# Kernel optimization log

Hardware: AMD Instinct MI355X
Metric: run time of the kernel (lower is better)

Reference implementation:

```python
import jax, jax.numpy as jnp
import numpy as np
import math

T, B, D = 1024, 256, 64
E, H, L = 512, 256, 4


def setup_inputs() -> dict:
    key = jax.random.key(0)
    ks = jax.random.split(key, 10)
    x_sequence = jax.random.normal(ks[0], (T, B, D), dtype=jnp.float32)
    seq_lengths = jax.random.randint(ks[1], (B,), 1, T)
    # create_b_mask: ones in first half of dims, zeros in second half
    b_mask = jnp.concatenate([jnp.ones((1, D // 2)), jnp.zeros((1, D // 2))], axis=1).astype(jnp.float32)
    W_in = jax.random.normal(ks[2], (L, D + E, H), dtype=jnp.float32) / np.sqrt(D + E)
    b_in = jnp.zeros((L, H), dtype=jnp.float32)
    W_s = jax.random.normal(ks[3], (L, H, D), dtype=jnp.float32) / np.sqrt(H)
    b_s = jnp.zeros((L, D), dtype=jnp.float32)
    W_t = jax.random.normal(ks[4], (L, H, D), dtype=jnp.float32) / np.sqrt(H)
    b_t = jnp.zeros((L, D), dtype=jnp.float32)
    rescale_w = jnp.ones((1, D), dtype=jnp.float32)
    # ESN reservoir (fixed random), scaled for spectral stability under tanh
    W_res = jax.random.normal(ks[5], (E, E), dtype=jnp.float32) * (0.9 / np.sqrt(E))
    W_inp = jax.random.normal(ks[6], (D, E), dtype=jnp.float32) * 0.1
    return dict(x_sequence=x_sequence, seq_lengths=seq_lengths, b_mask=b_mask,
                W_in=W_in, b_in=b_in, W_s=W_s, b_s=b_s, W_t=W_t, b_t=b_t,
                rescale_w=rescale_w, W_res=W_res, W_inp=W_inp)


def _forward(x_sequence, seq_lengths, b_mask, W_in, b_in, W_s, b_s, W_t, b_t,
             rescale_w, W_res, W_inp):
    Tlen, Bsz, Dd = x_sequence.shape
    log2pi = jnp.asarray(math.log(2.0 * math.pi), dtype=x_sequence.dtype)

    def nn_apply(xm, h_esn, l):
        # small conditioning MLP: concat(masked frame, esn state) -> hidden -> (slope, intercept)
        inp = jnp.concatenate([xm, h_esn], axis=1)           # (B, D+E)
        hid = jnp.tanh(inp @ W_in[l] + b_in[l])              # (B, H)
        slope = jnp.tanh(hid @ W_s[l] + b_s[l]) * rescale_w  # (B, D), rescaled
        intercept = hid @ W_t[l] + b_t[l]                    # (B, D)
        return slope, intercept

    def f_inverse(z, m, h_esn, l):
        slope, intercept = nn_apply(m * z, h_esn, l)
        z_new = m * z + (1.0 - m) * ((z - intercept) * jnp.exp(-slope))
        log_det = slope @ (m.T - 1.0)                        # (B, 1)
        return z_new, log_det

    def loglike_frame(x_frame, h_esn):
        ll = jnp.zeros((Bsz, 1), dtype=x_frame.dtype)
        z = x_frame
        for l in reversed(range(L)):  # small fixed loop over flow layers
            z, ld = f_inverse(z, 1.0 - b_mask, h_esn, l)
            ll = ll + ld
            z, ld = f_inverse(z, b_mask, h_esn, l)
            ll = ll + ld
        ll = ll - 0.5 * jnp.sum(z * z, axis=1, keepdims=True) - 0.5 * Dd * log2pi
        return ll

    def step(carry, inp):
        h_esn, ll_seq = carry
        t, x_frame = inp
        lf = loglike_frame(x_frame, h_esn)
        length_mask = (t < seq_lengths).astype(lf.dtype)[:, None]  # (B,1)
        ll_seq = ll_seq + lf * length_mask
        h_esn = jnp.tanh(h_esn @ W_res.T + x_frame @ W_inp)        # ESN update
        return (h_esn, ll_seq), None

    h0 = jnp.zeros((Bsz, W_res.shape[0]), dtype=x_sequence.dtype)
    ll0 = jnp.zeros((Bsz, 1), dtype=x_sequence.dtype)
    ts = jnp.arange(Tlen)
    (h_final, ll_seq), _ = jax.lax.scan(step, (h0, ll0), (ts, x_sequence))
    return ll_seq  # (B, 1)


def reference(x_sequence, seq_lengths, b_mask, W_in, b_in, W_s, b_s, W_t, b_t,
              rescale_w, W_res, W_inp):
    return _forward(x_sequence, seq_lengths, b_mask, W_in, b_in, W_s, b_s,
                    W_t, b_t, rescale_w, W_res, W_inp)
```

## Files before the change

kernel.cpp:

```cpp
#include <hip/hip_runtime.h>

#define T_LEN 1024
#define B_SZ  256
#define D_DIM 64
#define E_DIM 512
#define H_DIM 256

#define SA 552
#define SH 264
#define SF 66
#define ROWB 1152

using short8 = __attribute__((ext_vector_type(8))) short;
using half8  = __attribute__((ext_vector_type(8))) _Float16;
using f32x4  = __attribute__((ext_vector_type(4))) float;
typedef unsigned long long ull;

static __device__ __forceinline__ unsigned short f2bf(float v) {
    unsigned u = __float_as_uint(v);
    u += 0x7FFFu + ((u >> 16) & 1u);
    return (unsigned short)(u >> 16);
}
static __device__ __forceinline__ unsigned short f2h(float v) {
    _Float16 h = (_Float16)v;
    unsigned short u;
    __builtin_memcpy(&u, &h, 2);
    return u;
}
static __device__ __forceinline__ float h2f(unsigned short u) {
    _Float16 h;
    __builtin_memcpy(&h, &u, 2);
    return (float)h;
}
static __device__ __forceinline__ float fast_tanh(float x) {
    x = fminf(15.f, fmaxf(-15.f, x));
    float e = __expf(2.f * x);
    return (e - 1.f) / (e + 1.f);
}
static __device__ __forceinline__ int rswz(int row, int byte_in_row) {
    return row * ROWB + (byte_in_row ^ ((row & 7) << 4));
}

__global__ void prep_kernel(const float* __restrict__ W_in, const float* __restrict__ W_s,
                            const float* __restrict__ W_t, const float* __restrict__ W_res,
                            const float* __restrict__ W_inp, const float* __restrict__ x_seq,
                            unsigned short* __restrict__ W_inF, unsigned short* __restrict__ W_stF,
                            unsigned short* __restrict__ W_packo, unsigned short* __restrict__ x_h) {
    int idx = blockIdx.x * blockDim.x + threadIdx.x;
    int stride = gridDim.x * blockDim.x;
    const int total1 = 8 * 16 * 17 * 64 * 8;
    for (int i = idx; i < total1; i += stride) {
        int j    = i & 7;
        int lane = (i >> 3) & 63;
        int ks   = (i >> 9) % 17;
        int nt   = (i / (512 * 17)) & 15;
        int ls   = i / (512 * 17 * 16);
        int side = ls & 1, l = ls >> 1;
        int n = nt * 16 + (lane & 15);
        int k = ks * 32 + (lane >> 4) * 8 + j;
        int ksrc = (k < 32) ? (side == 0 ? 32 + k : k) : (k + 32);
        W_inF[i] = f2bf(W_in[(l * 576 + ksrc) * H_DIM + n]);
    }
    const int total2 = 8 * 4 * 8 * 64 * 8;
    for (int i = idx; i < total2; i += stride) {
        int j    = i & 7;
        int lane = (i >> 3) & 63;
        int ks   = (i >> 9) & 7;
        int nt   = (i >> 12) & 3;
        int ls   = i >> 14;
        int side = ls & 1, l = ls >> 1;
        int nst = nt * 16 + (lane & 15);
        int k   = ks * 32 + (lane >> 4) * 8 + j;
        int j32 = nst & 31;
        int d   = side ? (32 + j32) : j32;
        float v = (nst < 32) ? W_s[(l * H_DIM + k) * D_DIM + d] : W_t[(l * H_DIM + k) * D_DIM + d];
        W_stF[i] = f2bf(v);
    }
    const int total3 = E_DIM * 576;
    for (int i = idx; i < total3; i += stride) {
        int k = i % 576;
        int n = i / 576;
        float v = (k < E_DIM) ? W_res[n * E_DIM + k] : W_inp[(k - E_DIM) * E_DIM + n];
        W_packo[i] = f2h(v);
    }
    const int total4 = T_LEN * B_SZ * D_DIM;
    for (int i = idx; i < total4; i += stride)
        x_h[i] = f2h(x_seq[i]);
}

__launch_bounds__(256, 1)
__global__ void esn_kernel(const unsigned short* __restrict__ x_h,
                           const unsigned short* __restrict__ W_pack,
                           unsigned short* __restrict__ h_store ,
                           unsigned short* __restrict__ h_buf   ,
                           unsigned int* __restrict__ ctr,
                           int t0, int tc) {
    const int bid  = blockIdx.x;
    const int g    = bid & 15;
    const int m    = bid >> 4;
    const int tid  = threadIdx.x;
    const int wave = tid >> 6;
    const int lane = tid & 63;
    const int arow = lane & 15;
    const int kq   = lane >> 4;
    const int r0   = g * 16;
    const int n0   = m * 64;
    const size_t HB = (size_t)B_SZ * E_DIM;
    unsigned int* gctr = ctr + g * 32;

    extern __shared__ char smem[];
    char* Wlb = smem;
    char* hAb = smem + 64 * ROWB;

    {
        const int r  = tid & 63;
        const int c0 = (tid >> 6) * 18;
        #pragma unroll
        for (int u = 0; u < 18; ++u) {
            const int byte = 16 * (c0 + u);
            *reinterpret_cast<uint4*>(Wlb + rswz(r, byte)) =
                *reinterpret_cast<const uint4*>(
                    reinterpret_cast<const char*>(&W_pack[(size_t)(n0 + r) * 576]) + byte);
        }
    }

    const int srow = tid >> 4;
    const int seg  = tid & 15;
    const int xrow = tid >> 2, xc = tid & 3;

    for (int tl = 0; tl < tc; ++tl) {
        const int t = t0 + tl;
        const unsigned short* hb_r = h_buf + (size_t)(t & 1) * HB;
        unsigned short*       hb_w = h_buf + (size_t)((t & 1) ^ 1) * HB;

        uint4 xa = {0,0,0,0}, xb = {0,0,0,0};
        if (tid < 64) {
            const unsigned short* xp = &x_h[((size_t)t * B_SZ + r0 + xrow) * D_DIM + xc * 16];
            xa = *reinterpret_cast<const uint4*>(xp);
            xb = *reinterpret_cast<const uint4*>(xp + 8);
        }

        if (tid == 0) {
            while (__hip_atomic_fetch_add(gctr, 0u, __ATOMIC_RELAXED,
                                          __HIP_MEMORY_SCOPE_AGENT) < 8u * (unsigned)t)
                __builtin_amdgcn_s_sleep(1);
        }
        __syncthreads();
        asm volatile("" ::: "memory");

        ull hv[8];
        const ull* hrow = reinterpret_cast<const ull*>(&hb_r[(size_t)(r0 + srow) * E_DIM]);
        #pragma unroll
        for (int q = 0; q < 4; ++q) {
            const int c = seg + 16 * q;
            hv[2*q]   = __hip_atomic_load(hrow + 2*c,     __ATOMIC_RELAXED, __HIP_MEMORY_SCOPE_SYSTEM);
            hv[2*q+1] = __hip_atomic_load(hrow + 2*c + 1, __ATOMIC_RELAXED, __HIP_MEMORY_SCOPE_SYSTEM);
        }
        #pragma unroll
        for (int q = 0; q < 4; ++q) {
            const int c = seg + 16 * q;
            uint4 pk;
            __builtin_memcpy(&pk, &hv[2*q], 16);
            *reinterpret_cast<uint4*>(hAb + rswz(srow, 16 * c)) = pk;
        }
        if (tid < 64) {
            *reinterpret_cast<uint4*>(hAb + rswz(xrow, 1024 + 32 * xc))      = xa;
            *reinterpret_cast<uint4*>(hAb + rswz(xrow, 1024 + 32 * xc + 16)) = xb;
        }
        __syncthreads();

        if (tl == 0) {
            #pragma unroll
            for (int q = 0; q < 4; ++q) {
                const int c = seg + 16 * q;
                unsigned short o[8];
                #pragma unroll
                for (int j = 0; j < 4; ++j) o[j]     = f2bf(h2f((unsigned short)(hv[2*q]   >> (16 * j))));
                #pragma unroll
                for (int j = 0; j < 4; ++j) o[4 + j] = f2bf(h2f((unsigned short)(hv[2*q+1] >> (16 * j))));
                uint4 pk;
                __builtin_memcpy(&pk, o, 16);
                *reinterpret_cast<uint4*>(&h_store[(size_t)(r0 + srow) * E_DIM + 8 * c]) = pk;
            }
        }

        f32x4 accA = (f32x4){0.f, 0.f, 0.f, 0.f};
        f32x4 accB = (f32x4){0.f, 0.f, 0.f, 0.f};
        #pragma unroll
        for (int ks = 0; ks < 18; ++ks) {
            half8 a = *reinterpret_cast<const half8*>(hAb + rswz(arow, ks * 64 + kq * 16));
            half8 b = *reinterpret_cast<const half8*>(Wlb + rswz(wave * 16 + arow, ks * 64 + kq * 16));
            if (ks & 1) accB = __builtin_amdgcn_mfma_f32_16x16x32_f16(a, b, accB, 0, 0, 0);
            else        accA = __builtin_amdgcn_mfma_f32_16x16x32_f16(a, b, accA, 0, 0, 0);
        }
        f32x4 acc = accA + accB;

        const int ncol = n0 + wave * 16 + arow;
        #pragma unroll
        for (int i = 0; i < 4; ++i) {
            const int row = r0 + kq * 4 + i;
            float hvf = fast_tanh(acc[i]);
            __hip_atomic_store(&hb_w[(size_t)row * E_DIM + ncol], f2h(hvf),
                               __ATOMIC_RELAXED, __HIP_MEMORY_SCOPE_SYSTEM);
            if (tl + 1 < tc)
                h_store[((size_t)(tl + 1) * B_SZ + row) * E_DIM + ncol] = f2bf(hvf);
        }

        asm volatile("s_waitcnt vmcnt(0)" ::: "memory");
        __syncthreads();
        if (tid == 0)
            __hip_atomic_fetch_add(gctr, 1u, __ATOMIC_RELAXED, __HIP_MEMORY_SCOPE_AGENT);
    }
}

__launch_bounds__(256, 2)
__global__ void flow_kernel(const float* __restrict__ x_seq, const unsigned short* __restrict__ h_store,
                            const unsigned short* __restrict__ W_inF, const unsigned short* __restrict__ W_stF,
                            const float* __restrict__ b_in, const float* __restrict__ b_s,
                            const float* __restrict__ b_t, const float* __restrict__ rescale_w,
                            const int* __restrict__ seq_len, float* __restrict__ ll_part,
                            int t0, int tc) {
    const int tt   = blockIdx.x >> 4;
    const int bt   = blockIdx.x & 15;
    const int tid  = threadIdx.x;
    const int wave = tid >> 6;
    const int lane = tid & 63;

    __shared__ unsigned short abf[32 * SA];
    __shared__ unsigned short hidbf[32 * SH];
    __shared__ float zf[32][D_DIM];
    __shared__ float llacc[32];
    __shared__ float llb[16];
    float* stf = reinterpret_cast<float*>(hidbf);

    if (tid < 16) llb[tid] = 0.f;

    const int r8 = tid >> 3;
    const int c8 = tid & 7;

    for (int s = 0; s < 8; ++s) {
        const int trow = tt * 16 + 2 * s + (r8 >> 4);
        const int brow = bt * 16 + (r8 & 15);
        {
            const float* xp = &x_seq[((size_t)(t0 + trow) * B_SZ + brow) * D_DIM + c8 * 8];
            float4 v0 = *reinterpret_cast<const float4*>(xp);
            float4 v1 = *reinterpret_cast<const float4*>(xp + 4);
            *reinterpret_cast<float4*>(&zf[r8][c8 * 8])     = v0;
            *reinterpret_cast<float4*>(&zf[r8][c8 * 8 + 4]) = v1;
            const unsigned short* hp = &h_store[((size_t)trow * B_SZ + brow) * E_DIM + c8 * 64];
            unsigned short* ap = &abf[r8 * SA + 32 + c8 * 64];
            #pragma unroll
            for (int q = 0; q < 8; ++q)
                *reinterpret_cast<uint4*>(ap + q * 8) = *reinterpret_cast<const uint4*>(hp + q * 8);
        }
        if (tid < 32) llacc[tid] = 0.f;
        __syncthreads();

        for (int stage = 0; stage < 8; ++stage) {
            const int l = 3 - (stage >> 1);
            const int side = stage & 1;
            const int ls = l * 2 + side;
            {
                #pragma unroll
                for (int q = 0; q < 4; ++q) {
                    int k = c8 * 4 + q;
                    int d = side ? k : (32 + k);
                    abf[r8 * SA + k] = f2bf(zf[r8][d]);
                }
            }
            __syncthreads();

            const unsigned short* wbase =
                W_inF + ((size_t)(ls * 16 + wave * 4) * 17) * 512 + lane * 8;
            f32x4 acc[2][4];
            #pragma unroll
            for (int mt = 0; mt < 2; ++mt)
                #pragma unroll
                for (int nt = 0; nt < 4; ++nt)
                    acc[mt][nt] = (f32x4){0.f, 0.f, 0.f, 0.f};
            const int aoff = (lane & 15) * SA + 8 * (lane >> 4);
            short8 bb[6][4];
            #pragma unroll
            for (int p = 0; p < 6; ++p)
                #pragma unroll
                for (int nt = 0; nt < 4; ++nt)
                    bb[p][nt] = *reinterpret_cast<const short8*>(wbase + (size_t)nt * 8704 + p * 512);
            #pragma unroll
            for (int ks = 0; ks < 17; ++ks) {
                const int k0 = ks * 32;
                short8 a0 = *reinterpret_cast<const short8*>(&abf[aoff + k0]);
                short8 a1 = *reinterpret_cast<const short8*>(&abf[16 * SA + aoff + k0]);
                #pragma unroll
                for (int nt = 0; nt < 4; ++nt) {
                    acc[0][nt] = __builtin_amdgcn_mfma_f32_16x16x32_bf16(a0, bb[ks % 6][nt], acc[0][nt], 0, 0, 0);
                    acc[1][nt] = __builtin_amdgcn_mfma_f32_16x16x32_bf16(a1, bb[ks % 6][nt], acc[1][nt], 0, 0, 0);
                }
                if (ks + 6 < 17) {
                    #pragma unroll
                    for (int nt = 0; nt < 4; ++nt)
                        bb[ks % 6][nt] = *reinterpret_cast<const short8*>(
                            wbase + (size_t)nt * 8704 + (ks + 6) * 512);
                }
            }
            #pragma unroll
            for (int mt = 0; mt < 2; ++mt)
                #pragma unroll
                for (int nt = 0; nt < 4; ++nt) {
                    const int n = wave * 64 + nt * 16 + (lane & 15);
                    const float bias = b_in[l * H_DIM + n];
                    #pragma unroll
                    for (int i = 0; i < 4; ++i) {
                        const int row = mt * 16 + (lane >> 4) * 4 + i;
                        hidbf[row * SH + n] = f2bf(fast_tanh(acc[mt][nt][i] + bias));
                    }
                }
            __syncthreads();

            const unsigned short* wstb =
                W_stF + ((size_t)(ls * 4 + wave) * 8) * 512 + lane * 8;
            f32x4 acc2[2];
            acc2[0] = (f32x4){0.f,0.f,0.f,0.f};
            acc2[1] = (f32x4){0.f,0.f,0.f,0.f};
            const int hoff = (lane & 15) * SH + 8 * (lane >> 4);
            const int nst  = wave * 16 + (lane & 15);
            short8 bs0 = *reinterpret_cast<const short8*>(wstb);
            #pragma unroll
            for (int ks = 0; ks < 8; ++ks) {
                short8 bcur = bs0;
                if (ks + 1 < 8) bs0 = *reinterpret_cast<const short8*>(wstb + (ks + 1) * 512);
                const int k0 = ks * 32;
                short8 a0 = *reinterpret_cast<const short8*>(&hidbf[hoff + k0]);
                short8 a1 = *reinterpret_cast<const short8*>(&hidbf[16 * SH + hoff + k0]);
                acc2[0] = __builtin_amdgcn_mfma_f32_16x16x32_bf16(a0, bcur, acc2[0], 0, 0, 0);
                acc2[1] = __builtin_amdgcn_mfma_f32_16x16x32_bf16(a1, bcur, acc2[1], 0, 0, 0);
            }
            __syncthreads();
            {
                const int j = nst & 31;
                const int d = side ? (32 + j) : j;
                const bool is_s = (nst < 32);
                const float bias = is_s ? b_s[l * D_DIM + d] : b_t[l * D_DIM + d];
                const float rs = rescale_w[d];
                #pragma unroll
                for (int mt = 0; mt < 2; ++mt)
                    #pragma unroll
                    for (int i = 0; i < 4; ++i) {
                        const int row = mt * 16 + (lane >> 4) * 4 + i;
                        const float v = acc2[mt][i] + bias;
                        stf[row * SF + nst] = is_s ? (fast_tanh(v) * rs) : v;
                    }
            }
            __syncthreads();
            {
                float p = 0.f;
                #pragma unroll
                for (int q = 0; q < 4; ++q) {
                    const int j = c8 * 4 + q;
                    const int d = side ? (32 + j) : j;
                    const float sv = stf[r8 * SF + j];
                    const float iv = stf[r8 * SF + 32 + j];
                    zf[r8][d] = (zf[r8][d] - iv) * __expf(-sv);
                    p += sv;
                }
                p += __shfl_xor(p, 1);
                p += __shfl_xor(p, 2);
                p += __shfl_xor(p, 4);
                if (c8 == 0) llacc[r8] -= p;
            }
            __syncthreads();
        }

        {
            float zs = 0.f;
            #pragma unroll
            for (int q = 0; q < 8; ++q) {
                float z = zf[r8][c8 * 8 + q];
                zs += z * z;
            }
            zs += __shfl_xor(zs, 1);
            zs += __shfl_xor(zs, 2);
            zs += __shfl_xor(zs, 4);
            if (c8 == 0) {
                float ll = llacc[r8] - 0.5f * zs - 58.812066125f;
                llacc[r8] = ((t0 + trow) < seq_len[brow]) ? ll : 0.f;
            }
        }
        __syncthreads();
        if (tid < 16) llb[tid] += llacc[tid] + llacc[16 + tid];
        __syncthreads();
    }

    if (tid < 16)
        ll_part[((t0 >> 4) + tt) * B_SZ + bt * 16 + tid] = llb[tid];
}

__global__ void reduce_kernel(const float* __restrict__ ll_part, float* __restrict__ out) {
    int b = threadIdx.x;
    float s = 0.f;
    #pragma unroll
    for (int tt = 0; tt < T_LEN / 16; ++tt) s += ll_part[tt * B_SZ + b];
    out[b] = s;
}

extern "C" void kernel_launch(void* const* d_in, const int* in_sizes, int n_in,
                              void* d_out, int out_size, void* d_ws, size_t ws_size,
                              hipStream_t stream) {
    const float* x_seq   = (const float*)d_in[0];
    const int*   seqlen  = (const int*)d_in[1];
    const float* W_in    = (const float*)d_in[3];
    const float* b_in    = (const float*)d_in[4];
    const float* W_s     = (const float*)d_in[5];
    const float* b_s     = (const float*)d_in[6];
    const float* W_t     = (const float*)d_in[7];
    const float* b_t     = (const float*)d_in[8];
    const float* rescale = (const float*)d_in[9];
    const float* W_res   = (const float*)d_in[10];
    const float* W_inp   = (const float*)d_in[11];

    char* ws = (char*)d_ws;
    size_t off = 0;
    unsigned short* W_inF  = (unsigned short*)(ws + off); off += (size_t)8 * 16 * 17 * 64 * 8 * 2;
    unsigned short* W_stF  = (unsigned short*)(ws + off); off += (size_t)8 * 4 * 8 * 64 * 8 * 2;
    unsigned short* W_pack = (unsigned short*)(ws + off); off += (size_t)E_DIM * 576 * 2;
    unsigned short* x_h    = (unsigned short*)(ws + off); off += (size_t)T_LEN * B_SZ * D_DIM * 2;
    float* ll_part = (float*)(ws + off); off += (size_t)(T_LEN / 16) * B_SZ * 4;
    unsigned short* h_buf  = (unsigned short*)(ws + off); off += (size_t)2 * B_SZ * E_DIM * 2;
    unsigned int* ctr = (unsigned int*)(ws + off); off += (size_t)16 * 32 * 4;
    unsigned short* h_store = (unsigned short*)(ws + off);

    size_t per_t = (size_t)B_SZ * E_DIM * 2;
    size_t rem = (ws_size > off) ? (ws_size - off) : 0;
    long long tcl = (long long)(rem / per_t);
    int tc = (int)((tcl > T_LEN) ? T_LEN : tcl);
    tc &= ~15;
    if (tc < 16) tc = 16;

    hipMemsetAsync(h_buf, 0, (size_t)2 * B_SZ * E_DIM * 2, stream);
    hipMemsetAsync(ctr, 0, (size_t)16 * 32 * 4, stream);

    prep_kernel<<<2048, 256, 0, stream>>>(W_in, W_s, W_t, W_res, W_inp, x_seq,
                                          W_inF, W_stF, W_pack, x_h);
    const int esn_lds = (64 + 16) * ROWB;
    for (int t0 = 0; t0 < T_LEN; t0 += tc) {
        int cur = T_LEN - t0; if (cur > tc) cur = tc;
        esn_kernel<<<128, 256, esn_lds, stream>>>(x_h, W_pack, h_store, h_buf, ctr, t0, cur);
        flow_kernel<<<(cur / 16) * 16, 256, 0, stream>>>(x_seq, h_store, W_inF, W_stF, b_in, b_s, b_t,
                                                         rescale, seqlen, ll_part, t0, cur);
    }
    reduce_kernel<<<1, B_SZ, 0, stream>>>(ll_part, (float*)d_out);
}
```

Measured before the change: 3.851 ms.

## Process 64 rows per flow-kernel iteration to amortize weight fetches

Result: slower. 4.833 ms (+25.5%).

```diff
diff --git a/kernel.cpp b/kernel.cpp
--- a/kernel.cpp
+++ b/kernel.cpp
@@ -10,6 +10,8 @@
 #define SH 264
 #define SF 66
 #define ROWB 1152
+
+#define FLOW_LDS (64*SA*2 + 64*SH*2 + 64*64*4 + 64*4 + 16*4)
 
 using short8 = __attribute__((ext_vector_type(8))) short;
 using half8  = __attribute__((ext_vector_type(8))) _Float16;
@@ -213,7 +215,7 @@
     }
 }
 
-__launch_bounds__(256, 2)
+__launch_bounds__(256, 1)
 __global__ void flow_kernel(const float* __restrict__ x_seq, const unsigned short* __restrict__ h_store,
                             const unsigned short* __restrict__ W_inF, const unsigned short* __restrict__ W_stF,
                             const float* __restrict__ b_in, const float* __restrict__ b_s,
@@ -226,34 +228,35 @@
     const int wave = tid >> 6;
     const int lane = tid & 63;
 
-    __shared__ unsigned short abf[32 * SA];
-    __shared__ unsigned short hidbf[32 * SH];
-    __shared__ float zf[32][D_DIM];
-    __shared__ float llacc[32];
-    __shared__ float llb[16];
-    float* stf = reinterpret_cast<float*>(hidbf);
+    extern __shared__ char smemf[];
+    unsigned short* abf   = reinterpret_cast<unsigned short*>(smemf);
+    unsigned short* hidbf = abf + 64 * SA;
+    float* zf    = reinterpret_cast<float*>(hidbf + 64 * SH);
+    float* llacc = zf + 64 * 64;
+    float* llb   = llacc + 64;
+    float* stf   = reinterpret_cast<float*>(hidbf);
 
     if (tid < 16) llb[tid] = 0.f;
 
-    const int r8 = tid >> 3;
-    const int c8 = tid & 7;
-
-    for (int s = 0; s < 8; ++s) {
-        const int trow = tt * 16 + 2 * s + (r8 >> 4);
-        const int brow = bt * 16 + (r8 & 15);
+    const int row4 = tid >> 2;
+    const int c4   = tid & 3;
+
+    for (int s = 0; s < 4; ++s) {
+        const int trow = tt * 16 + 4 * s + (row4 >> 4);
+        const int brow = bt * 16 + (row4 & 15);
         {
-            const float* xp = &x_seq[((size_t)(t0 + trow) * B_SZ + brow) * D_DIM + c8 * 8];
-            float4 v0 = *reinterpret_cast<const float4*>(xp);
-            float4 v1 = *reinterpret_cast<const float4*>(xp + 4);
-            *reinterpret_cast<float4*>(&zf[r8][c8 * 8])     = v0;
-            *reinterpret_cast<float4*>(&zf[r8][c8 * 8 + 4]) = v1;
-            const unsigned short* hp = &h_store[((size_t)trow * B_SZ + brow) * E_DIM + c8 * 64];
-            unsigned short* ap = &abf[r8 * SA + 32 + c8 * 64];
-            #pragma unroll
-            for (int q = 0; q < 8; ++q)
+            const float* xp = &x_seq[((size_t)(t0 + trow) * B_SZ + brow) * D_DIM + c4 * 16];
+            #pragma unroll
+            for (int q = 0; q < 4; ++q)
+                *reinterpret_cast<float4*>(&zf[row4 * 64 + c4 * 16 + q * 4]) =
+                    *reinterpret_cast<const float4*>(xp + q * 4);
+            const unsigned short* hp = &h_store[((size_t)trow * B_SZ + brow) * E_DIM + c4 * 128];
+            unsigned short* ap = &abf[row4 * SA + 32 + c4 * 128];
+            #pragma unroll
+            for (int q = 0; q < 16; ++q)
                 *reinterpret_cast<uint4*>(ap + q * 8) = *reinterpret_cast<const uint4*>(hp + q * 8);
         }
-        if (tid < 32) llacc[tid] = 0.f;
+        if (tid < 64) llacc[tid] = 0.f;
         __syncthreads();
 
         for (int stage = 0; stage < 8; ++stage) {
@@ -262,19 +265,19 @@
             const int ls = l * 2 + side;
             {
                 #pragma unroll
-                for (int q = 0; q < 4; ++q) {
-                    int k = c8 * 4 + q;
+                for (int q = 0; q < 8; ++q) {
+                    int k = c4 * 8 + q;
                     int d = side ? k : (32 + k);
-                    abf[r8 * SA + k] = f2bf(zf[r8][d]);
+                    abf[row4 * SA + k] = f2bf(zf[row4 * 64 + d]);
                 }
             }
             __syncthreads();
 
             const unsigned short* wbase =
                 W_inF + ((size_t)(ls * 16 + wave * 4) * 17) * 512 + lane * 8;
-            f32x4 acc[2][4];
-            #pragma unroll
-            for (int mt = 0; mt < 2; ++mt)
+            f32x4 acc[4][4];
+            #pragma unroll
+            for (int mt = 0; mt < 4; ++mt)
                 #pragma unroll
                 for (int nt = 0; nt < 4; ++nt)
                     acc[mt][nt] = (f32x4){0.f, 0.f, 0.f, 0.f};
@@ -288,13 +291,15 @@
             #pragma unroll
             for (int ks = 0; ks < 17; ++ks) {
                 const int k0 = ks * 32;
-                short8 a0 = *reinterpret_cast<const short8*>(&abf[aoff + k0]);
-                short8 a1 = *reinterpret_cast<const short8*>(&abf[16 * SA + aoff + k0]);
-                #pragma unroll
-                for (int nt = 0; nt < 4; ++nt) {
-                    acc[0][nt] = __builtin_amdgcn_mfma_f32_16x16x32_bf16(a0, bb[ks % 6][nt], acc[0][nt], 0, 0, 0);
-                    acc[1][nt] = __builtin_amdgcn_mfma_f32_16x16x32_bf16(a1, bb[ks % 6][nt], acc[1][nt], 0, 0, 0);
-                }
+                short8 am[4];
+                #pragma unroll
+                for (int mt = 0; mt < 4; ++mt)
+                    am[mt] = *reinterpret_cast<const short8*>(&abf[mt * 16 * SA + aoff + k0]);
+                #pragma unroll
+                for (int nt = 0; nt < 4; ++nt)
+                    #pragma unroll
+                    for (int mt = 0; mt < 4; ++mt)
+                        acc[mt][nt] = __builtin_amdgcn_mfma_f32_16x16x32_bf16(am[mt], bb[ks % 6][nt], acc[mt][nt], 0, 0, 0);
                 if (ks + 6 < 17) {
                     #pragma unroll
                     for (int nt = 0; nt < 4; ++nt)
@@ -303,24 +308,24 @@
                 }
             }
             #pragma unroll
-            for (int mt = 0; mt < 2; ++mt)
-                #pragma unroll
-                for (int nt = 0; nt < 4; ++nt) {
-                    const int n = wave * 64 + nt * 16 + (lane & 15);
-                    const float bias = b_in[l * H_DIM + n];
+            for (int nt = 0; nt < 4; ++nt) {
+                const int n = wave * 64 + nt * 16 + (lane & 15);
+                const float bias = b_in[l * H_DIM + n];
+                #pragma unroll
+                for (int mt = 0; mt < 4; ++mt)
                     #pragma unroll
                     for (int i = 0; i < 4; ++i) {
                         const int row = mt * 16 + (lane >> 4) * 4 + i;
                         hidbf[row * SH + n] = f2bf(fast_tanh(acc[mt][nt][i] + bias));
                     }
-                }
+            }
             __syncthreads();
 
             const unsigned short* wstb =
                 W_stF + ((size_t)(ls * 4 + wave) * 8) * 512 + lane * 8;
-            f32x4 acc2[2];
-            acc2[0] = (f32x4){0.f,0.f,0.f,0.f};
-            acc2[1] = (f32x4){0.f,0.f,0.f,0.f};
+            f32x4 acc2[4];
+            #pragma unroll
+            for (int mt = 0; mt < 4; ++mt) acc2[mt] = (f32x4){0.f, 0.f, 0.f, 0.f};
             const int hoff = (lane & 15) * SH + 8 * (lane >> 4);
             const int nst  = wave * 16 + (lane & 15);
             short8 bs0 = *reinterpret_cast<const short8*>(wstb);
@@ -329,10 +334,11 @@
                 short8 bcur = bs0;
                 if (ks + 1 < 8) bs0 = *reinterpret_cast<const short8*>(wstb + (ks + 1) * 512);
                 const int k0 = ks * 32;
-                short8 a0 = *reinterpret_cast<const short8*>(&hidbf[hoff + k0]);
-                short8 a1 = *reinterpret_cast<const short8*>(&hidbf[16 * SH + hoff + k0]);
-                acc2[0] = __builtin_amdgcn_mfma_f32_16x16x32_bf16(a0, bcur, acc2[0], 0, 0, 0);
-                acc2[1] = __builtin_amdgcn_mfma_f32_16x16x32_bf16(a1, bcur, acc2[1], 0, 0, 0);
+                #pragma unroll
+                for (int mt = 0; mt < 4; ++mt) {
+                    short8 a = *reinterpret_cast<const short8*>(&hidbf[mt * 16 * SH + hoff + k0]);
+                    acc2[mt] = __builtin_amdgcn_mfma_f32_16x16x32_bf16(a, bcur, acc2[mt], 0, 0, 0);
+                }
             }
             __syncthreads();
             {
@@ -342,7 +348,7 @@
                 const float bias = is_s ? b_s[l * D_DIM + d] : b_t[l * D_DIM + d];
                 const float rs = rescale_w[d];
                 #pragma unroll
-                for (int mt = 0; mt < 2; ++mt)
+                for (int mt = 0; mt < 4; ++mt)
                     #pragma unroll
                     for (int i = 0; i < 4; ++i) {
                         const int row = mt * 16 + (lane >> 4) * 4 + i;
@@ -354,18 +360,17 @@
             {
                 float p = 0.f;
                 #pragma unroll
-                for (int q = 0; q < 4; ++q) {
-                    const int j = c8 * 4 + q;
+                for (int q = 0; q < 8; ++q) {
+                    const int j = c4 * 8 + q;
                     const int d = side ? (32 + j) : j;
-                    const float sv = stf[r8 * SF + j];
-                    const float iv = stf[r8 * SF + 32 + j];
-                    zf[r8][d] = (zf[r8][d] - iv) * __expf(-sv);
+                    const float sv = stf[row4 * SF + j];
+                    const float iv = stf[row4 * SF + 32 + j];
+                    zf[row4 * 64 + d] = (zf[row4 * 64 + d] - iv) * __expf(-sv);
                     p += sv;
                 }
                 p += __shfl_xor(p, 1);
                 p += __shfl_xor(p, 2);
-                p += __shfl_xor(p, 4);
-                if (c8 == 0) llacc[r8] -= p;
+                if (c4 == 0) llacc[row4] -= p;
             }
             __syncthreads();
         }
@@ -373,20 +378,20 @@
         {
             float zs = 0.f;
             #pragma unroll
-            for (int q = 0; q < 8; ++q) {
-                float z = zf[r8][c8 * 8 + q];
+            for (int q = 0; q < 16; ++q) {
+                float z = zf[row4 * 64 + c4 * 16 + q];
                 zs += z * z;
             }
             zs += __shfl_xor(zs, 1);
             zs += __shfl_xor(zs, 2);
-            zs += __shfl_xor(zs, 4);
-            if (c8 == 0) {
-                float ll = llacc[r8] - 0.5f * zs - 58.812066125f;
-                llacc[r8] = ((t0 + trow) < seq_len[brow]) ? ll : 0.f;
-            }
-        }
-        __syncthreads();
-        if (tid < 16) llb[tid] += llacc[tid] + llacc[16 + tid];
+            if (c4 == 0) {
+                float ll = llacc[row4] - 0.5f * zs - 58.812066125f;
+                llacc[row4] = ((t0 + trow) < seq_len[brow]) ? ll : 0.f;
+            }
+        }
+        __syncthreads();
+        if (tid < 16)
+            llb[tid] += llacc[tid] + llacc[16 + tid] + llacc[32 + tid] + llacc[48 + tid];
         __syncthreads();
     }
 
@@ -444,8 +449,9 @@
     for (int t0 = 0; t0 < T_LEN; t0 += tc) {
         int cur = T_LEN - t0; if (cur > tc) cur = tc;
         esn_kernel<<<128, 256, esn_lds, stream>>>(x_h, W_pack, h_store, h_buf, ctr, t0, cur);
-        flow_kernel<<<(cur / 16) * 16, 256, 0, stream>>>(x_seq, h_store, W_inF, W_stF, b_in, b_s, b_t,
-                                                         rescale, seqlen, ll_part, t0, cur);
+        flow_kernel<<<(cur / 16) * 16, 256, FLOW_LDS, stream>>>(x_seq, h_store, W_inF, W_stF,
+                                                                b_in, b_s, b_t, rescale, seqlen,
+                                                                ll_part, t0, cur);
     }
     reduce_kernel<<<1, B_SZ, 0, stream>>>(ll_part, (float*)d_out);
 }
```

## Restructure flow kernel to process four row-groups per stage and keep z in registers

Applied to the files above, without the earlier changes.

Result: slower. 4.005 ms (+4.0%).

```diff
diff --git a/kernel.cpp b/kernel.cpp
--- a/kernel.cpp
+++ b/kernel.cpp
@@ -10,6 +10,8 @@
 #define SH 264
 #define SF 66
 #define ROWB 1152
+
+#define FLOW_LDS (128*SA*2 + 32*SH*2 + 128*4)
 
 using short8 = __attribute__((ext_vector_type(8))) short;
 using half8  = __attribute__((ext_vector_type(8))) _Float16;
@@ -213,63 +215,68 @@
     }
 }
 
-__launch_bounds__(256, 2)
+__launch_bounds__(256, 1)
 __global__ void flow_kernel(const float* __restrict__ x_seq, const unsigned short* __restrict__ h_store,
                             const unsigned short* __restrict__ W_inF, const unsigned short* __restrict__ W_stF,
                             const float* __restrict__ b_in, const float* __restrict__ b_s,
                             const float* __restrict__ b_t, const float* __restrict__ rescale_w,
                             const int* __restrict__ seq_len, float* __restrict__ ll_part,
                             int t0, int tc) {
-    const int tt   = blockIdx.x >> 4;
+    const int ttb  = blockIdx.x >> 4;
     const int bt   = blockIdx.x & 15;
     const int tid  = threadIdx.x;
     const int wave = tid >> 6;
     const int lane = tid & 63;
 
-    __shared__ unsigned short abf[32 * SA];
-    __shared__ unsigned short hidbf[32 * SH];
-    __shared__ float zf[32][D_DIM];
-    __shared__ float llacc[32];
-    __shared__ float llb[16];
-    float* stf = reinterpret_cast<float*>(hidbf);
-
-    if (tid < 16) llb[tid] = 0.f;
+    extern __shared__ char smemf[];
+    unsigned short* abf   = reinterpret_cast<unsigned short*>(smemf);
+    unsigned short* hidbf = abf + 128 * SA;
+    float* llacc = reinterpret_cast<float*>(hidbf + 32 * SH);
+    float* stf   = reinterpret_cast<float*>(hidbf);
 
     const int r8 = tid >> 3;
     const int c8 = tid & 7;
 
-    for (int s = 0; s < 8; ++s) {
-        const int trow = tt * 16 + 2 * s + (r8 >> 4);
+    float z[4][8];
+    #pragma unroll
+    for (int s = 0; s < 4; ++s) {
+        const int trow = ttb * 8 + 2 * s + (r8 >> 4);
         const int brow = bt * 16 + (r8 & 15);
-        {
-            const float* xp = &x_seq[((size_t)(t0 + trow) * B_SZ + brow) * D_DIM + c8 * 8];
-            float4 v0 = *reinterpret_cast<const float4*>(xp);
-            float4 v1 = *reinterpret_cast<const float4*>(xp + 4);
-            *reinterpret_cast<float4*>(&zf[r8][c8 * 8])     = v0;
-            *reinterpret_cast<float4*>(&zf[r8][c8 * 8 + 4]) = v1;
-            const unsigned short* hp = &h_store[((size_t)trow * B_SZ + brow) * E_DIM + c8 * 64];
-            unsigned short* ap = &abf[r8 * SA + 32 + c8 * 64];
-            #pragma unroll
-            for (int q = 0; q < 8; ++q)
-                *reinterpret_cast<uint4*>(ap + q * 8) = *reinterpret_cast<const uint4*>(hp + q * 8);
-        }
-        if (tid < 32) llacc[tid] = 0.f;
-        __syncthreads();
-
-        for (int stage = 0; stage < 8; ++stage) {
-            const int l = 3 - (stage >> 1);
-            const int side = stage & 1;
-            const int ls = l * 2 + side;
+        const float* xp = &x_seq[((size_t)(t0 + trow) * B_SZ + brow) * D_DIM + c8 * 8];
+        float4 v0 = *reinterpret_cast<const float4*>(xp);
+        float4 v1 = *reinterpret_cast<const float4*>(xp + 4);
+        z[s][0] = v0.x; z[s][1] = v0.y; z[s][2] = v0.z; z[s][3] = v0.w;
+        z[s][4] = v1.x; z[s][5] = v1.y; z[s][6] = v1.z; z[s][7] = v1.w;
+        const unsigned short* hp = &h_store[((size_t)trow * B_SZ + brow) * E_DIM + c8 * 64];
+        unsigned short* ap = &abf[(s * 32 + r8) * SA + 32 + c8 * 64];
+        #pragma unroll
+        for (int q = 0; q < 8; ++q)
+            *reinterpret_cast<uint4*>(ap + q * 8) = *reinterpret_cast<const uint4*>(hp + q * 8);
+    }
+    if (tid < 128) llacc[tid] = 0.f;
+    __syncthreads();
+
+    for (int stage = 0; stage < 8; ++stage) {
+        const int l = 3 - (stage >> 1);
+        const int side = stage & 1;
+        const int ls = l * 2 + side;
+
+        for (int s = 0; s < 4; ++s) {
             {
-                #pragma unroll
-                for (int q = 0; q < 4; ++q) {
-                    int k = c8 * 4 + q;
-                    int d = side ? k : (32 + k);
-                    abf[r8 * SA + k] = f2bf(zf[r8][d]);
+                const bool act = side ? (c8 < 4) : (c8 >= 4);
+                if (act) {
+                    unsigned short o[8];
+                    #pragma unroll
+                    for (int q = 0; q < 8; ++q) o[q] = f2bf(z[s][q]);
+                    const int k = side ? (c8 * 8) : ((c8 - 4) * 8);
+                    uint4 pk;
+                    __builtin_memcpy(&pk, o, 16);
+                    *reinterpret_cast<uint4*>(&abf[(s * 32 + r8) * SA + k]) = pk;
                 }
             }
             __syncthreads();
 
+            const int base0 = s * 32 * SA;
             const unsigned short* wbase =
                 W_inF + ((size_t)(ls * 16 + wave * 4) * 17) * 512 + lane * 8;
             f32x4 acc[2][4];
@@ -288,8 +295,8 @@
             #pragma unroll
             for (int ks = 0; ks < 17; ++ks) {
                 const int k0 = ks * 32;
-                short8 a0 = *reinterpret_cast<const short8*>(&abf[aoff + k0]);
-                short8 a1 = *reinterpret_cast<const short8*>(&abf[16 * SA + aoff + k0]);
+                short8 a0 = *reinterpret_cast<const short8*>(&abf[base0 + aoff + k0]);
+                short8 a1 = *reinterpret_cast<const short8*>(&abf[base0 + 16 * SA + aoff + k0]);
                 #pragma unroll
                 for (int nt = 0; nt < 4; ++nt) {
                     acc[0][nt] = __builtin_amdgcn_mfma_f32_16x16x32_bf16(a0, bb[ks % 6][nt], acc[0][nt], 0, 0, 0);
@@ -352,53 +359,58 @@
             }
             __syncthreads();
             {
-                float p = 0.f;
-                #pragma unroll
-                for (int q = 0; q < 4; ++q) {
-                    const int j = c8 * 4 + q;
-                    const int d = side ? (32 + j) : j;
-                    const float sv = stf[r8 * SF + j];
-                    const float iv = stf[r8 * SF + 32 + j];
-                    zf[r8][d] = (zf[r8][d] - iv) * __expf(-sv);
-                    p += sv;
+                const bool act = side ? (c8 >= 4) : (c8 < 4);
+                if (act) {
+                    const int jb = (c8 & 3) * 8;
+                    float p = 0.f;
+                    #pragma unroll
+                    for (int q = 0; q < 8; ++q) {
+                        const float sv = stf[r8 * SF + jb + q];
+                        const float iv = stf[r8 * SF + 32 + jb + q];
+                        z[s][q] = (z[s][q] - iv) * __expf(-sv);
+                        p += sv;
+                    }
+                    p += __shfl_xor(p, 1);
+                    p += __shfl_xor(p, 2);
+                    if ((c8 & 3) == 0) llacc[s * 32 + r8] -= p;
                 }
-                p += __shfl_xor(p, 1);
-                p += __shfl_xor(p, 2);
-                p += __shfl_xor(p, 4);
-                if (c8 == 0) llacc[r8] -= p;
-            }
-            __syncthreads();
-        }
-
-        {
+            }
+        }
+    }
+
+    __syncthreads();
+    {
+        #pragma unroll
+        for (int s = 0; s < 4; ++s) {
             float zs = 0.f;
             #pragma unroll
-            for (int q = 0; q < 8; ++q) {
-                float z = zf[r8][c8 * 8 + q];
-                zs += z * z;
-            }
+            for (int q = 0; q < 8; ++q) zs += z[s][q] * z[s][q];
             zs += __shfl_xor(zs, 1);
             zs += __shfl_xor(zs, 2);
             zs += __shfl_xor(zs, 4);
             if (c8 == 0) {
-                float ll = llacc[r8] - 0.5f * zs - 58.812066125f;
-                llacc[r8] = ((t0 + trow) < seq_len[brow]) ? ll : 0.f;
-            }
-        }
-        __syncthreads();
-        if (tid < 16) llb[tid] += llacc[tid] + llacc[16 + tid];
-        __syncthreads();
-    }
-
-    if (tid < 16)
-        ll_part[((t0 >> 4) + tt) * B_SZ + bt * 16 + tid] = llb[tid];
+                const int trow = ttb * 8 + 2 * s + (r8 >> 4);
+                const int brow = bt * 16 + (r8 & 15);
+                float ll = llacc[s * 32 + r8] - 0.5f * zs - 58.812066125f;
+                llacc[s * 32 + r8] = ((t0 + trow) < seq_len[brow]) ? ll : 0.f;
+            }
+        }
+    }
+    __syncthreads();
+    if (tid < 16) {
+        float acc = 0.f;
+        #pragma unroll
+        for (int s = 0; s < 4; ++s)
+            acc += llacc[s * 32 + tid] + llacc[s * 32 + 16 + tid];
+        ll_part[((size_t)((t0 >> 3) + ttb)) * B_SZ + bt * 16 + tid] = acc;
+    }
 }
 
 __global__ void reduce_kernel(const float* __restrict__ ll_part, float* __restrict__ out) {
     int b = threadIdx.x;
     float s = 0.f;
     #pragma unroll
-    for (int tt = 0; tt < T_LEN / 16; ++tt) s += ll_part[tt * B_SZ + b];
+    for (int tt = 0; tt < T_LEN / 8; ++tt) s += ll_part[tt * B_SZ + b];
     out[b] = s;
 }
 
@@ -423,7 +435,7 @@
     unsigned short* W_stF  = (unsigned short*)(ws + off); off += (size_t)8 * 4 * 8 * 64 * 8 * 2;
     unsigned short* W_pack = (unsigned short*)(ws + off); off += (size_t)E_DIM * 576 * 2;
     unsigned short* x_h    = (unsigned short*)(ws + off); off += (size_t)T_LEN * B_SZ * D_DIM * 2;
-    float* ll_part = (float*)(ws + off); off += (size_t)(T_LEN / 16) * B_SZ * 4;
+    float* ll_part = (float*)(ws + off); off += (size_t)(T_LEN / 8) * B_SZ * 4;
     unsigned short* h_buf  = (unsigned short*)(ws + off); off += (size_t)2 * B_SZ * E_DIM * 2;
     unsigned int* ctr = (unsigned int*)(ws + off); off += (size_t)16 * 32 * 4;
     unsigned short* h_store = (unsigned short*)(ws + off);
@@ -444,8 +456,9 @@
     for (int t0 = 0; t0 < T_LEN; t0 += tc) {
         int cur = T_LEN - t0; if (cur > tc) cur = tc;
         esn_kernel<<<128, 256, esn_lds, stream>>>(x_h, W_pack, h_store, h_buf, ctr, t0, cur);
-        flow_kernel<<<(cur / 16) * 16, 256, 0, stream>>>(x_seq, h_store, W_inF, W_stF, b_in, b_s, b_t,
-                                                         rescale, seqlen, ll_part, t0, cur);
+        flow_kernel<<<(cur / 8) * 16, 256, FLOW_LDS, stream>>>(x_seq, h_store, W_inF, W_stF,
+                                                               b_in, b_s, b_t, rescale, seqlen,
+                                                               ll_part, t0, cur);
     }
     reduce_kernel<<<1, B_SZ, 0, stream>>>(ll_part, (float*)d_out);
 }
```
